# Optimization experiments

Hardware: AMD Instinct MI355X
Metric: run time of the kernel (lower is better)

Reference implementation:

```python
import jax, jax.numpy as jnp
import numpy as np

D = 768      # hidden_size
H = 12       # num_attention_heads
HD = D // H  # head_dim
F = 3072     # intermediate_size
B, S = 4, 2048
EPS = 1e-5


def _layer_norm(x, g, b):
    mu = jnp.mean(x, axis=-1, keepdims=True)
    var = jnp.mean(jnp.square(x - mu), axis=-1, keepdims=True)
    return (x - mu) * jax.lax.rsqrt(var + EPS) * g + b


def setup_inputs() -> dict:
    key = jax.random.key(0)
    ks = jax.random.split(key, 12)
    s_d = 1.0 / np.sqrt(D)
    s_f = 1.0 / np.sqrt(F)
    return {
        "x": jax.random.normal(ks[0], (B, S, D), jnp.float32),
        # per-head separate Q/K/V projections stacked along head axis [H, D, HD]
        "Wq": jax.random.normal(ks[1], (H, D, HD), jnp.float32) * s_d,
        "bq": jnp.zeros((H, HD), jnp.float32),
        "Wk": jax.random.normal(ks[2], (H, D, HD), jnp.float32) * s_d,
        "bk": jnp.zeros((H, HD), jnp.float32),
        "Wv": jax.random.normal(ks[3], (H, D, HD), jnp.float32) * s_d,
        "bv": jnp.zeros((H, HD), jnp.float32),
        "Wo": jax.random.normal(ks[4], (D, D), jnp.float32) * s_d,
        "bo": jnp.zeros((D,), jnp.float32),
        "W1": jax.random.normal(ks[5], (D, F), jnp.float32) * s_d,
        "b1": jnp.zeros((F,), jnp.float32),
        "W2": jax.random.normal(ks[6], (F, D), jnp.float32) * s_f,
        "b2": jnp.zeros((D,), jnp.float32),
        "g1": jnp.ones((D,), jnp.float32),
        "be1": jnp.zeros((D,), jnp.float32),
        "g2": jnp.ones((D,), jnp.float32),
        "be2": jnp.zeros((D,), jnp.float32),
    }


def reference(x, Wq, bq, Wk, bk, Wv, bv, Wo, bo, W1, b1, W2, b2, g1, be1, g2, be2):
    # NOTE: original module has NO residual connections; mask path is a no-op
    # (masked_fill is not in-place in the source), dropout is identity in eval.
    h = _layer_norm(x, g1, be1)
    # per-head projections: [B,H,S,HD]
    q = jnp.einsum('bsd,hde->bhse', h, Wq) + bq[None, :, None, :]
    k = jnp.einsum('bsd,hde->bhse', h, Wk) + bk[None, :, None, :]
    v = jnp.einsum('bsd,hde->bhse', h, Wv) + bv[None, :, None, :]
    scores = jnp.einsum('bhse,bhte->bhst', q, k) / jnp.sqrt(jnp.float32(HD))
    w = jax.nn.softmax(scores, axis=-1)          # [B,H,S,S]
    o = jnp.einsum('bhst,bhte->bhse', w, v)      # [B,H,S,HD]
    o = o.transpose(0, 2, 1, 3).reshape(B, S, D)  # concat heads along feature dim
    a = o @ Wo + bo
    h2 = _layer_norm(a, g2, be2)
    f = jax.nn.gelu(h2 @ W1 + b1, approximate=False)  # torch nn.GELU = exact erf
    return f @ W2 + b2
```

## Files before the change

### kernel.cpp

```cpp
#include <hip/hip_runtime.h>
#include <hip/hip_bf16.h>
#include <math.h>

typedef __hip_bfloat16 bf16;
typedef __attribute__((ext_vector_type(8))) short short8;
typedef __attribute__((ext_vector_type(4))) float f32x4;

#define D_  768
#define H_  12
#define HD_ 64
#define F_  3072
#define B_  4
#define S_  2048
#define BS_ (B_*S_)
#define SQK 1536
#define PSTR 72

__device__ __forceinline__ float b2f(bf16 x){ return __bfloat162float(x); }

union BU { bf16 b; unsigned short u; };
__device__ __forceinline__ bf16 f2b_fast(float x){
  BU t; t.u = (unsigned short)((__float_as_uint(x) + 0x8000u) >> 16); return t.b;
}
__device__ __forceinline__ unsigned pk2bf(float a, float b){
  return __builtin_amdgcn_perm(__float_as_uint(b) + 0x8000u,
                               __float_as_uint(a) + 0x8000u, 0x07060302u);
}

__device__ __forceinline__ f32x4 zero4(){ f32x4 z; z.x=0.f; z.y=0.f; z.z=0.f; z.w=0.f; return z; }

__device__ __forceinline__ f32x4 mfma16(uint4 a, uint4 b, f32x4 c){
  union U { uint4 u; short8 s; };
  U A, B; A.u = a; B.u = b;
  return __builtin_amdgcn_mfma_f32_16x16x32_bf16(A.s, B.s, c, 0, 0, 0);
}

typedef const __attribute__((address_space(1))) void gvoid;
typedef __attribute__((address_space(3))) void lvoid;
__device__ __forceinline__ void load_lds16(const void* g, void* l){
  __builtin_amdgcn_global_load_lds((gvoid*)g, (lvoid*)l, 16, 0, 0);
}

__device__ __forceinline__ float fast_gelu(float v){
  const float x = v * 0.70710678118654752f;
  const float ax = fabsf(x);
  const float t = __builtin_amdgcn_rcpf(fmaf(0.3275911f, ax, 1.0f));
  const float poly = t * fmaf(t, fmaf(t, fmaf(t, fmaf(t, 1.061405429f, -1.453152027f),
                                              1.421413741f), -0.284496736f), 0.254829592f);
  const float e = __builtin_amdgcn_exp2f(ax * ax * -1.4426950408889634f);
  const float erfax = 1.0f - poly * e;
  const float erfx = copysignf(erfax, x);
  return 0.5f * v * (1.0f + erfx);
}

__global__ __launch_bounds__(256)
void repack_t(const float* __restrict__ W, bf16* __restrict__ Wt, int K, int N)
{
  const int t = blockIdx.x * 256 + threadIdx.x;
  const int n = t % N;
  const int kg = t / N;
  const float* src = W + (size_t)kg * 8 * N + n;
  union { unsigned u32[4]; uint4 u; } pk;
#pragma unroll
  for (int j = 0; j < 4; ++j)
    pk.u32[j] = pk2bf(src[(size_t)(2 * j) * N], src[(size_t)(2 * j + 1) * N]);
  *(uint4*)(Wt + ((size_t)n * (K >> 3) + kg) * 8) = pk.u;
}

__global__ __launch_bounds__(256)
void repack_qkv_t(const float* __restrict__ Wq, const float* __restrict__ Wk,
                  const float* __restrict__ Wv, bf16* __restrict__ Wt)
{
  const int t = blockIdx.x * 256 + threadIdx.x;
  const int n = t % 2304;
  const int kg = t / 2304;
  const int sel = n / 768;
  const int nn = n - sel * 768;
  const int hh = nn >> 6;
  const int ee = nn & 63;
  const float* W = (sel == 0) ? Wq : (sel == 1) ? Wk : Wv;
  const float* src = W + ((size_t)hh * 768 + (size_t)kg * 8) * 64 + ee;
  union { unsigned u32[4]; uint4 u; } pk;
#pragma unroll
  for (int j = 0; j < 4; ++j)
    pk.u32[j] = pk2bf(src[(size_t)(2 * j) * 64], src[(size_t)(2 * j + 1) * 64]);
  *(uint4*)(Wt + ((size_t)n * 96 + kg) * 8) = pk.u;
}

__global__ __launch_bounds__(256)
void bias_qkv(const float* __restrict__ bq, const float* __restrict__ bk,
              const float* __restrict__ bv, float* __restrict__ out)
{
  const int t = blockIdx.x * 256 + threadIdx.x;
  out[t] = (t < 768) ? bq[t] : (t < 1536) ? bk[t - 768] : bv[t - 1536];
}

__global__ __launch_bounds__(256)
void ln_x_kernel(const float* __restrict__ X, const float* __restrict__ G,
                 const float* __restrict__ Bet, bf16* __restrict__ Y)
{
  const int t = threadIdx.x;
  const size_t row = blockIdx.x;
  const float* x = X + row * D_;
  float v0 = x[t], v1 = x[t + 256], v2 = x[t + 512];
  float s = v0 + v1 + v2;
#pragma unroll
  for (int d = 32; d >= 1; d >>= 1) s += __shfl_xor(s, d, 64);
  __shared__ float red[8];
  const int wv = t >> 6, ln = t & 63;
  if (ln == 0) red[wv] = s;
  __syncthreads();
  const float mu = (red[0] + red[1] + red[2] + red[3]) * (1.0f / 768.0f);
  const float d0 = v0 - mu, d1 = v1 - mu, d2 = v2 - mu;
  float sq = d0 * d0 + d1 * d1 + d2 * d2;
#pragma unroll
  for (int d = 32; d >= 1; d >>= 1) sq += __shfl_xor(sq, d, 64);
  if (ln == 0) red[4 + wv] = sq;
  __syncthreads();
  const float var = (red[4] + red[5] + red[6] + red[7]) * (1.0f / 768.0f);
  const float rs = rsqrtf(var + 1e-5f);
  bf16* y = Y + row * D_;
  y[t]       = f2b_fast(d0 * rs * G[t]       + Bet[t]);
  y[t + 256] = f2b_fast(d1 * rs * G[t + 256] + Bet[t + 256]);
  y[t + 512] = f2b_fast(d2 * rs * G[t + 512] + Bet[t + 512]);
}

__global__ __launch_bounds__(256)
void ln_h_kernel(const bf16* __restrict__ X, const float* __restrict__ G,
                 const float* __restrict__ Bet, bf16* __restrict__ Y)
{
  const int t = threadIdx.x;
  const size_t row = blockIdx.x;
  const bf16* x = X + row * D_;
  float v0 = b2f(x[t]), v1 = b2f(x[t + 256]), v2 = b2f(x[t + 512]);
  float s = v0 + v1 + v2;
#pragma unroll
  for (int d = 32; d >= 1; d >>= 1) s += __shfl_xor(s, d, 64);
  __shared__ float red[8];
  const int wv = t >> 6, ln = t & 63;
  if (ln == 0) red[wv] = s;
  __syncthreads();
  const float mu = (red[0] + red[1] + red[2] + red[3]) * (1.0f / 768.0f);
  const float d0 = v0 - mu, d1 = v1 - mu, d2 = v2 - mu;
  float sq = d0 * d0 + d1 * d1 + d2 * d2;
#pragma unroll
  for (int d = 32; d >= 1; d >>= 1) sq += __shfl_xor(sq, d, 64);
  if (ln == 0) red[4 + wv] = sq;
  __syncthreads();
  const float var = (red[4] + red[5] + red[6] + red[7]) * (1.0f / 768.0f);
  const float rs = rsqrtf(var + 1e-5f);
  bf16* y = Y + row * D_;
  y[t]       = f2b_fast(d0 * rs * G[t]       + Bet[t]);
  y[t + 256] = f2b_fast(d1 * rs * G[t + 256] + Bet[t + 256]);
  y[t + 512] = f2b_fast(d2 * rs * G[t + 512] + Bet[t + 512]);
}

__global__ __launch_bounds__(256)
void gemm_lds(const bf16* __restrict__ A, const bf16* __restrict__ Wt,
              const float* __restrict__ bias, bf16* __restrict__ C,
              bf16* __restrict__ Vp, float* __restrict__ Cf,
              int K, int N, int mode)
{
  __shared__ __align__(16) bf16 As[2][128 * 32];
  __shared__ __align__(16) bf16 Bs[2][128 * 32];

  const int tid = threadIdx.x;
  const int wave = tid >> 6, lane = tid & 63;
  const int l15 = lane & 15, qd = lane >> 4;
  const int wy = wave >> 1, wx = wave & 1;

  int id = (int)blockIdx.y * (int)gridDim.x + (int)blockIdx.x;
  const int chunk = ((int)gridDim.x * (int)gridDim.y) >> 3;
  id = (id & 7) * chunk + (id >> 3);
  const int bx = id % (int)gridDim.x;
  const int by = id / (int)gridDim.x;

  const size_t m0 = (size_t)by * 128;
  const int n0 = bx * 128;

  const int r0 = tid >> 2, c0 = tid & 3;
  const int c0s = c0 ^ ((r0 >> 1) & 3);
  const bf16* Ag0 = A  + (m0 + r0) * (size_t)K + c0s * 8;
  const bf16* Ag1 = A  + (m0 + r0 + 64) * (size_t)K + c0s * 8;
  const bf16* Bg0 = Wt + (size_t)(n0 + r0) * K + c0s * 8;
  const bf16* Bg1 = Wt + (size_t)(n0 + r0 + 64) * K + c0s * 8;

  f32x4 acc[4][4];
#pragma unroll
  for (int i = 0; i < 4; ++i)
#pragma unroll
    for (int j = 0; j < 4; ++j) acc[i][j] = zero4();

  const int arow = wy * 64;
  const int brow = wx * 64;
  const int ksw = (l15 >> 1) & 3;

  load_lds16(Ag0, &As[0][(size_t)tid * 8]);
  load_lds16(Ag1, &As[0][(size_t)(tid + 256) * 8]);
  load_lds16(Bg0, &Bs[0][(size_t)tid * 8]);
  load_lds16(Bg1, &Bs[0][(size_t)(tid + 256) * 8]);
  __syncthreads();

  for (int k0 = 0; k0 < K; k0 += 32) {
    const int cur = (k0 >> 5) & 1;
    if (k0 + 32 < K) {
      const int nxt = cur ^ 1;
      load_lds16(Ag0 + k0 + 32, &As[nxt][(size_t)tid * 8]);
      load_lds16(Ag1 + k0 + 32, &As[nxt][(size_t)(tid + 256) * 8]);
      load_lds16(Bg0 + k0 + 32, &Bs[nxt][(size_t)tid * 8]);
      load_lds16(Bg1 + k0 + 32, &Bs[nxt][(size_t)(tid + 256) * 8]);
    }
    uint4 af[4], bfr[4];
#pragma unroll
    for (int mt = 0; mt < 4; ++mt)
      af[mt] = *(const uint4*)(&As[cur][0] + (size_t)(arow + mt * 16 + l15) * 32 + (qd ^ ksw) * 8);
#pragma unroll
    for (int nt = 0; nt < 4; ++nt)
      bfr[nt] = *(const uint4*)(&Bs[cur][0] + (size_t)(brow + nt * 16 + l15) * 32 + (qd ^ ksw) * 8);
#pragma unroll
    for (int nt = 0; nt < 4; ++nt)
#pragma unroll
      for (int mt = 0; mt < 4; ++mt)
        acc[nt][mt] = mfma16(bfr[nt], af[mt], acc[nt][mt]);
    __syncthreads();
  }

  const size_t wm0 = m0 + arow;
  const int wn0 = n0 + brow;
#pragma unroll
  for (int nt = 0; nt < 4; ++nt) {
    const int nb = wn0 + nt * 16 + qd * 4;
    const f32x4 bs4 = *(const f32x4*)(bias + nb);
#pragma unroll
    for (int mt = 0; mt < 4; ++mt) {
      const size_t m = wm0 + mt * 16 + l15;
      float v[4];
#pragma unroll
      for (int r = 0; r < 4; ++r) v[r] = acc[nt][mt][r] + bs4[r];
      if (mode == 2) {
#pragma unroll
        for (int r = 0; r < 4; ++r) v[r] = fast_gelu(v[r]);
      }
      if (mode == 3) {
        f32x4 o; o.x = v[0]; o.y = v[1]; o.z = v[2]; o.w = v[3];
        *(f32x4*)(Cf + m * (size_t)N + nb) = o;
      } else if (mode == 0) {
        if (nb < SQK) {
          uint2 w; w.x = pk2bf(v[0], v[1]); w.y = pk2bf(v[2], v[3]);
          *(uint2*)(C + m * SQK + nb) = w;
        } else {
          const int bb = (int)(m >> 11);
          const int ss = (int)(m & 2047);
          const int hh = (nb - SQK) >> 6;
          const size_t vbase = (((size_t)bb * H_ + hh) * 256 + (ss >> 3)) * 512 + (ss & 7);
#pragma unroll
          for (int r = 0; r < 4; ++r)
            Vp[vbase + (size_t)((nb & 63) + r) * 8] = f2b_fast(v[r]);
        }
      } else {
        uint2 w; w.x = pk2bf(v[0], v[1]); w.y = pk2bf(v[2], v[3]);
        *(uint2*)(C + m * (size_t)N + nb) = w;
      }
    }
  }
}

__global__ __launch_bounds__(256)
void gemm_lds64(const bf16* __restrict__ A, const bf16* __restrict__ Wt,
                const float* __restrict__ bias, bf16* __restrict__ C,
                float* __restrict__ Cf, int K, int N, int mode)
{
  __shared__ __align__(16) bf16 As[2][128 * 32];
  __shared__ __align__(16) bf16 Bs[2][64 * 32];

  const int tid = threadIdx.x;
  const int wave = tid >> 6, lane = tid & 63;
  const int l15 = lane & 15, qd = lane >> 4;

  int id = (int)blockIdx.y * (int)gridDim.x + (int)blockIdx.x;
  const int chunk = ((int)gridDim.x * (int)gridDim.y) >> 3;
  id = (id & 7) * chunk + (id >> 3);
  const int bx = id % (int)gridDim.x;
  const int by = id / (int)gridDim.x;

  const size_t m0 = (size_t)by * 128;
  const int n0 = bx * 64;

  const int r0 = tid >> 2, c0 = tid & 3;
  const int c0s = c0 ^ ((r0 >> 1) & 3);
  const bf16* Ag0 = A  + (m0 + r0) * (size_t)K + c0s * 8;
  const bf16* Ag1 = A  + (m0 + r0 + 64) * (size_t)K + c0s * 8;
  const bf16* Bg0 = Wt + (size_t)(n0 + r0) * K + c0s * 8;

  f32x4 acc[4][2];
#pragma unroll
  for (int i = 0; i < 4; ++i)
#pragma unroll
    for (int j = 0; j < 2; ++j) acc[i][j] = zero4();

  const int arow = wave * 32;
  const int ksw = (l15 >> 1) & 3;

  load_lds16(Ag0, &As[0][(size_t)tid * 8]);
  load_lds16(Ag1, &As[0][(size_t)(tid + 256) * 8]);
  load_lds16(Bg0, &Bs[0][(size_t)tid * 8]);
  __syncthreads();

  for (int k0 = 0; k0 < K; k0 += 32) {
    const int cur = (k0 >> 5) & 1;
    if (k0 + 32 < K) {
      const int nxt = cur ^ 1;
      load_lds16(Ag0 + k0 + 32, &As[nxt][(size_t)tid * 8]);
      load_lds16(Ag1 + k0 + 32, &As[nxt][(size_t)(tid + 256) * 8]);
      load_lds16(Bg0 + k0 + 32, &Bs[nxt][(size_t)tid * 8]);
    }
    uint4 af[2], bfr[4];
#pragma unroll
    for (int mt = 0; mt < 2; ++mt)
      af[mt] = *(const uint4*)(&As[cur][0] + (size_t)(arow + mt * 16 + l15) * 32 + (qd ^ ksw) * 8);
#pragma unroll
    for (int nt = 0; nt < 4; ++nt)
      bfr[nt] = *(const uint4*)(&Bs[cur][0] + (size_t)(nt * 16 + l15) * 32 + (qd ^ ksw) * 8);
#pragma unroll
    for (int nt = 0; nt < 4; ++nt)
#pragma unroll
      for (int mt = 0; mt < 2; ++mt)
        acc[nt][mt] = mfma16(bfr[nt], af[mt], acc[nt][mt]);
    __syncthreads();
  }

  const size_t wm0 = m0 + arow;
#pragma unroll
  for (int nt = 0; nt < 4; ++nt) {
    const int nb = n0 + nt * 16 + qd * 4;
    const f32x4 bs4 = *(const f32x4*)(bias + nb);
#pragma unroll
    for (int mt = 0; mt < 2; ++mt) {
      const size_t m = wm0 + mt * 16 + l15;
      float v[4];
#pragma unroll
      for (int r = 0; r < 4; ++r) v[r] = acc[nt][mt][r] + bs4[r];
      if (mode == 3) {
        f32x4 o; o.x = v[0]; o.y = v[1]; o.z = v[2]; o.w = v[3];
        *(f32x4*)(Cf + m * (size_t)N + nb) = o;
      } else {
        uint2 w; w.x = pk2bf(v[0], v[1]); w.y = pk2bf(v[2], v[3]);
        *(uint2*)(C + m * (size_t)N + nb) = w;
      }
    }
  }
}

__global__ __launch_bounds__(256, 3)
void attn_kernel(const bf16* __restrict__ QK, const bf16* __restrict__ Vp,
                 bf16* __restrict__ O)
{
  const int tid  = threadIdx.x;
  const int wave = tid >> 6;
  const int lane = tid & 63;
  const int l15 = lane & 15;
  const int qd  = lane >> 4;

  int bid = blockIdx.y * gridDim.x + blockIdx.x;
  bid = (bid & 7) * 96 + (bid >> 3);
  const int bh = bid >> 4;
  const int b  = bh / H_;
  const int h  = bh % H_;
  const int q0 = (bid & 15) * 128 + wave * 32;

  const bf16* Qb = QK + (size_t)b * S_ * SQK + h * HD_;
  const bf16* Kb = Qb + D_;
  const bf16* Vb = Vp + (size_t)bh * 256 * 512;

  __shared__ __align__(16) bf16 Ks[2][64 * 64];
  __shared__ __align__(16) bf16 Vs[2][8 * 512];
  __shared__ __align__(16) unsigned short Pl[4][32 * PSTR];
  unsigned short* Pw = &Pl[wave][0];

  const int srow = tid >> 3;
  const int sch  = (tid & 7) ^ (srow & 7);
  const bf16* Kst = Kb + (size_t)srow * SQK + sch * 8;
  const bf16* Vst = Vb + tid * 8;

  uint4 qf[2][2];
#pragma unroll
  for (int mt = 0; mt < 2; ++mt)
#pragma unroll
    for (int ks = 0; ks < 2; ++ks)
      qf[mt][ks] = *(const uint4*)(Qb + (size_t)(q0 + mt * 16 + l15) * SQK + ks * 32 + qd * 8);

  f32x4 o_[2][5];
#pragma unroll
  for (int mt = 0; mt < 2; ++mt)
#pragma unroll
    for (int dt = 0; dt < 5; ++dt) o_[mt][dt] = zero4();

  uint4 vones;
  { const unsigned v = (l15 == 0) ? 0x3F803F80u : 0u; vones.x = v; vones.y = v; vones.z = v; vones.w = v; }

  const float C1 = 1.4426950408889634f * 0.125f;
  const float C0 = -12.0f * 1.4426950408889634f;

  load_lds16(Kst,                      &Ks[0][tid * 8]);
  load_lds16(Kst + (size_t)32 * SQK,   &Ks[0][2048 + tid * 8]);
  load_lds16(Vst,                      &Vs[0][tid * 8]);
  load_lds16(Vst + 2048,               &Vs[0][2048 + tid * 8]);
  __syncthreads();

  for (int sk = 0; sk < S_; sk += 64) {
    const int cur = (sk >> 6) & 1;
    const bf16* Ksc = &Ks[cur][0];
    const bf16* Vsc = &Vs[cur][0];

    uint4 kf[4][2];
#pragma unroll
    for (int kt = 0; kt < 4; ++kt)
#pragma unroll
      for (int ks = 0; ks < 2; ++ks)
        kf[kt][ks] = *(const uint4*)(Ksc + (size_t)(kt * 16 + l15) * 64
                                         + ((ks * 4 + qd) ^ (l15 & 7)) * 8);
    uint4 vf[2][4];
#pragma unroll
    for (int ks = 0; ks < 2; ++ks)
#pragma unroll
      for (int dt = 0; dt < 4; ++dt)
        vf[ks][dt] = *(const uint4*)(Vsc + (ks * 4 + qd) * 512 + (dt * 16 + l15) * 8);

    if (sk + 64 < S_) {
      const int nxt = cur ^ 1;
      const bf16* Kn = Kst + (size_t)(sk + 64) * SQK;
      const bf16* Vn = Vst + (size_t)(sk + 64) * 64;
      load_lds16(Kn,                    &Ks[nxt][tid * 8]);
      load_lds16(Kn + (size_t)32 * SQK, &Ks[nxt][2048 + tid * 8]);
      load_lds16(Vn,                    &Vs[nxt][tid * 8]);
      load_lds16(Vn + 2048,             &Vs[nxt][2048 + tid * 8]);
    }

    f32x4 st[4][2];
#pragma unroll
    for (int kt = 0; kt < 4; ++kt)
#pragma unroll
      for (int mt = 0; mt < 2; ++mt) st[kt][mt] = zero4();
    __builtin_amdgcn_s_setprio(1);
#pragma unroll
    for (int ks = 0; ks < 2; ++ks)
#pragma unroll
      for (int kt = 0; kt < 4; ++kt)
#pragma unroll
        for (int mt = 0; mt < 2; ++mt)
          st[kt][mt] = mfma16(kf[kt][ks], qf[mt][ks], st[kt][mt]);
    __builtin_amdgcn_s_setprio(0);

#pragma unroll
    for (int mt = 0; mt < 2; ++mt) {
      unsigned short* prow = Pw + (mt * 16 + l15) * PSTR;
#pragma unroll
      for (int kt = 0; kt < 4; ++kt) {
        const float p0 = __builtin_amdgcn_exp2f(fmaf(st[kt][mt][0], C1, C0));
        const float p1 = __builtin_amdgcn_exp2f(fmaf(st[kt][mt][1], C1, C0));
        const float p2 = __builtin_amdgcn_exp2f(fmaf(st[kt][mt][2], C1, C0));
        const float p3 = __builtin_amdgcn_exp2f(fmaf(st[kt][mt][3], C1, C0));
        uint2 w; w.x = pk2bf(p0, p1); w.y = pk2bf(p2, p3);
        *(uint2*)(prow + kt * 16 + qd * 4) = w;
      }
    }

    uint4 pf[2][2];
#pragma unroll
    for (int mt = 0; mt < 2; ++mt)
#pragma unroll
      for (int ks = 0; ks < 2; ++ks)
        pf[mt][ks] = *(const uint4*)(Pw + (mt * 16 + l15) * PSTR + ks * 32 + qd * 8);

    __builtin_amdgcn_s_setprio(1);
#pragma unroll
    for (int ks = 0; ks < 2; ++ks)
#pragma unroll
      for (int mt = 0; mt < 2; ++mt) {
#pragma unroll
        for (int dt = 0; dt < 4; ++dt)
          o_[mt][dt] = mfma16(pf[mt][ks], vf[ks][dt], o_[mt][dt]);
        o_[mt][4] = mfma16(pf[mt][ks], vones, o_[mt][4]);
      }
    __builtin_amdgcn_s_setprio(0);

    __syncthreads();
  }

  const size_t tok0 = (size_t)b * S_ + q0;
#pragma unroll
  for (int mt = 0; mt < 2; ++mt) {
#pragma unroll
    for (int r = 0; r < 4; ++r) {
      const float lr = __shfl(o_[mt][4][r], (lane & 48), 64);
      const float inv = __builtin_amdgcn_rcpf(lr);
      const size_t row = tok0 + mt * 16 + qd * 4 + r;
#pragma unroll
      for (int dt = 0; dt < 4; ++dt)
        O[row * D_ + h * HD_ + dt * 16 + l15] = f2b_fast(o_[mt][dt][r] * inv);
    }
  }
}

extern "C" void kernel_launch(void* const* d_in, const int* in_sizes, int n_in,
                              void* d_out, int out_size, void* d_ws, size_t ws_size,
                              hipStream_t stream)
{
  const float* x   = (const float*)d_in[0];
  const float* Wq  = (const float*)d_in[1];
  const float* bq  = (const float*)d_in[2];
  const float* Wk  = (const float*)d_in[3];
  const float* bk  = (const float*)d_in[4];
  const float* Wv  = (const float*)d_in[5];
  const float* bv  = (const float*)d_in[6];
  const float* Wo  = (const float*)d_in[7];
  const float* bo  = (const float*)d_in[8];
  const float* W1  = (const float*)d_in[9];
  const float* b1  = (const float*)d_in[10];
  const float* W2  = (const float*)d_in[11];
  const float* b2  = (const float*)d_in[12];
  const float* g1  = (const float*)d_in[13];
  const float* be1 = (const float*)d_in[14];
  const float* g2  = (const float*)d_in[15];
  const float* be2 = (const float*)d_in[16];

  const bool full = ws_size >= (size_t)77079552;

  char* ws = (char*)d_ws;
  bf16* qk     = (bf16*)(ws + 0);
  bf16* vp     = (bf16*)(ws + 25165824);
  bf16* h1     = (bf16*)(ws + 37748736);
  bf16* obuf   = h1;
  bf16* abuf   = (bf16*)(ws + 0);
  bf16* h2     = (bf16*)(ws + (full ? 50331648u : 25165824u));
  bf16* fbuf   = (bf16*)(ws + 0);
  const size_t wb = full ? 62914560u : 50331648u;
  bf16* wqkv_p = (bf16*)(ws + wb);
  bf16* wo_p   = (bf16*)(ws + wb + 3538944u);
  bf16* w1_p   = (bf16*)(ws + wb + 4718592u);
  bf16* w2_p   = (bf16*)(ws + wb + 9437184u);
  float* bqkvf = (float*)(ws + wb + 14155776u);

  float* outp = (float*)d_out;

  repack_qkv_t<<<dim3(864),  dim3(256), 0, stream>>>(Wq, Wk, Wv, wqkv_p);
  repack_t    <<<dim3(288),  dim3(256), 0, stream>>>(Wo, wo_p, 768, 768);
  repack_t    <<<dim3(1152), dim3(256), 0, stream>>>(W1, w1_p, 768, 3072);
  repack_t    <<<dim3(1152), dim3(256), 0, stream>>>(W2, w2_p, 3072, 768);
  bias_qkv    <<<dim3(9),    dim3(256), 0, stream>>>(bq, bk, bv, bqkvf);

  ln_x_kernel<<<dim3(BS_), dim3(256), 0, stream>>>(x, g1, be1, h1);
  gemm_lds<<<dim3(18, 64), dim3(256), 0, stream>>>(h1, wqkv_p, bqkvf, qk, vp, nullptr, 768, 2304, 0);
  attn_kernel<<<dim3(16, 48), dim3(256), 0, stream>>>(qk, vp, obuf);
  gemm_lds64<<<dim3(12, 64), dim3(256), 0, stream>>>(obuf, wo_p, bo, abuf, nullptr, 768, 768, 1);
  ln_h_kernel<<<dim3(BS_), dim3(256), 0, stream>>>(abuf, g2, be2, h2);

  if (full) {
    gemm_lds<<<dim3(24, 64), dim3(256), 0, stream>>>(h2, w1_p, b1, fbuf, nullptr, nullptr, 768, 3072, 2);
    gemm_lds64<<<dim3(12, 64), dim3(256), 0, stream>>>(fbuf, w2_p, b2, nullptr, outp, 3072, 768, 3);
  } else {
    gemm_lds<<<dim3(24, 32), dim3(256), 0, stream>>>(h2, w1_p, b1, fbuf, nullptr, nullptr, 768, 3072, 2);
    gemm_lds64<<<dim3(12, 32), dim3(256), 0, stream>>>(fbuf, w2_p, b2, nullptr, outp, 3072, 768, 3);
    gemm_lds<<<dim3(24, 32), dim3(256), 0, stream>>>(h2 + (size_t)4096 * D_, w1_p, b1, fbuf, nullptr, nullptr, 768, 3072, 2);
    gemm_lds64<<<dim3(12, 32), dim3(256), 0, stream>>>(fbuf, w2_p, b2, nullptr, outp + (size_t)4096 * D_, 3072, 768, 3);
  }
}
```

Baseline: 421.0 us.

## Deepen K-tile to 64 in narrow GEMM and hoist LDS fragment reads before prefetch

The 128x64 GEMM kernel now stages 64-wide K slices per iteration instead of 32, using an 8-chunk XOR swizzle and double-buffered shared memory that is twice as large. This halves the number of barrier-separated iterations and issues more MFMAs per sync. In both GEMM kernels the LDS fragment reads are moved ahead of the next-tile global-to-LDS prefetch so they are not queued behind it. The larger shared footprint may reduce occupancy.

```diff
diff --git a/kernel.cpp b/kernel.cpp
--- a/kernel.cpp
+++ b/kernel.cpp
@@ -203,6 +203,13 @@
 
   for (int k0 = 0; k0 < K; k0 += 32) {
     const int cur = (k0 >> 5) & 1;
+    uint4 af[4], bfr[4];
+#pragma unroll
+    for (int mt = 0; mt < 4; ++mt)
+      af[mt] = *(const uint4*)(&As[cur][0] + (size_t)(arow + mt * 16 + l15) * 32 + (qd ^ ksw) * 8);
+#pragma unroll
+    for (int nt = 0; nt < 4; ++nt)
+      bfr[nt] = *(const uint4*)(&Bs[cur][0] + (size_t)(brow + nt * 16 + l15) * 32 + (qd ^ ksw) * 8);
     if (k0 + 32 < K) {
       const int nxt = cur ^ 1;
       load_lds16(Ag0 + k0 + 32, &As[nxt][(size_t)tid * 8]);
@@ -210,13 +217,6 @@
       load_lds16(Bg0 + k0 + 32, &Bs[nxt][(size_t)tid * 8]);
       load_lds16(Bg1 + k0 + 32, &Bs[nxt][(size_t)(tid + 256) * 8]);
     }
-    uint4 af[4], bfr[4];
-#pragma unroll
-    for (int mt = 0; mt < 4; ++mt)
-      af[mt] = *(const uint4*)(&As[cur][0] + (size_t)(arow + mt * 16 + l15) * 32 + (qd ^ ksw) * 8);
-#pragma unroll
-    for (int nt = 0; nt < 4; ++nt)
-      bfr[nt] = *(const uint4*)(&Bs[cur][0] + (size_t)(brow + nt * 16 + l15) * 32 + (qd ^ ksw) * 8);
 #pragma unroll
     for (int nt = 0; nt < 4; ++nt)
 #pragma unroll
@@ -270,8 +270,8 @@
                 const float* __restrict__ bias, bf16* __restrict__ C,
                 float* __restrict__ Cf, int K, int N, int mode)
 {
-  __shared__ __align__(16) bf16 As[2][128 * 32];
-  __shared__ __align__(16) bf16 Bs[2][64 * 32];
+  __shared__ __align__(16) bf16 As[2][128 * 64];
+  __shared__ __align__(16) bf16 Bs[2][64 * 64];
 
   const int tid = threadIdx.x;
   const int wave = tid >> 6, lane = tid & 63;
@@ -286,11 +286,10 @@
   const size_t m0 = (size_t)by * 128;
   const int n0 = bx * 64;
 
-  const int r0 = tid >> 2, c0 = tid & 3;
-  const int c0s = c0 ^ ((r0 >> 1) & 3);
-  const bf16* Ag0 = A  + (m0 + r0) * (size_t)K + c0s * 8;
-  const bf16* Ag1 = A  + (m0 + r0 + 64) * (size_t)K + c0s * 8;
-  const bf16* Bg0 = Wt + (size_t)(n0 + r0) * K + c0s * 8;
+  const int srow = tid >> 3;
+  const int sch  = (tid & 7) ^ (srow & 7);
+  const bf16* Ag = A  + (m0 + srow) * (size_t)K + sch * 8;
+  const bf16* Bg = Wt + (size_t)(n0 + srow) * K + sch * 8;
 
   f32x4 acc[4][2];
 #pragma unroll
@@ -299,33 +298,47 @@
     for (int j = 0; j < 2; ++j) acc[i][j] = zero4();
 
   const int arow = wave * 32;
-  const int ksw = (l15 >> 1) & 3;
-
-  load_lds16(Ag0, &As[0][(size_t)tid * 8]);
-  load_lds16(Ag1, &As[0][(size_t)(tid + 256) * 8]);
-  load_lds16(Bg0, &Bs[0][(size_t)tid * 8]);
-  __syncthreads();
-
-  for (int k0 = 0; k0 < K; k0 += 32) {
-    const int cur = (k0 >> 5) & 1;
-    if (k0 + 32 < K) {
+  const int ksw = l15 & 7;
+
+#pragma unroll
+  for (int p = 0; p < 4; ++p)
+    load_lds16(Ag + (size_t)32 * p * K, &As[0][(size_t)(tid + 256 * p) * 8]);
+#pragma unroll
+  for (int p = 0; p < 2; ++p)
+    load_lds16(Bg + (size_t)32 * p * K, &Bs[0][(size_t)(tid + 256 * p) * 8]);
+  __syncthreads();
+
+  for (int k0 = 0; k0 < K; k0 += 64) {
+    const int cur = (k0 >> 6) & 1;
+    uint4 af[2][2], bfr[4][2];
+#pragma unroll
+    for (int mt = 0; mt < 2; ++mt)
+#pragma unroll
+      for (int ks = 0; ks < 2; ++ks)
+        af[mt][ks] = *(const uint4*)(&As[cur][0]
+                       + (size_t)(arow + mt * 16 + l15) * 64 + ((ks * 4 + qd) ^ ksw) * 8);
+#pragma unroll
+    for (int nt = 0; nt < 4; ++nt)
+#pragma unroll
+      for (int ks = 0; ks < 2; ++ks)
+        bfr[nt][ks] = *(const uint4*)(&Bs[cur][0]
+                       + (size_t)(nt * 16 + l15) * 64 + ((ks * 4 + qd) ^ ksw) * 8);
+    if (k0 + 64 < K) {
       const int nxt = cur ^ 1;
-      load_lds16(Ag0 + k0 + 32, &As[nxt][(size_t)tid * 8]);
-      load_lds16(Ag1 + k0 + 32, &As[nxt][(size_t)(tid + 256) * 8]);
-      load_lds16(Bg0 + k0 + 32, &Bs[nxt][(size_t)tid * 8]);
-    }
-    uint4 af[2], bfr[4];
-#pragma unroll
-    for (int mt = 0; mt < 2; ++mt)
-      af[mt] = *(const uint4*)(&As[cur][0] + (size_t)(arow + mt * 16 + l15) * 32 + (qd ^ ksw) * 8);
-#pragma unroll
-    for (int nt = 0; nt < 4; ++nt)
-      bfr[nt] = *(const uint4*)(&Bs[cur][0] + (size_t)(nt * 16 + l15) * 32 + (qd ^ ksw) * 8);
-#pragma unroll
-    for (int nt = 0; nt < 4; ++nt)
-#pragma unroll
-      for (int mt = 0; mt < 2; ++mt)
-        acc[nt][mt] = mfma16(bfr[nt], af[mt], acc[nt][mt]);
+#pragma unroll
+      for (int p = 0; p < 4; ++p)
+        load_lds16(Ag + (size_t)32 * p * K + k0 + 64, &As[nxt][(size_t)(tid + 256 * p) * 8]);
+#pragma unroll
+      for (int p = 0; p < 2; ++p)
+        load_lds16(Bg + (size_t)32 * p * K + k0 + 64, &Bs[nxt][(size_t)(tid + 256 * p) * 8]);
+    }
+#pragma unroll
+    for (int ks = 0; ks < 2; ++ks)
+#pragma unroll
+      for (int nt = 0; nt < 4; ++nt)
+#pragma unroll
+        for (int mt = 0; mt < 2; ++mt)
+          acc[nt][mt] = mfma16(bfr[nt][ks], af[mt][ks], acc[nt][mt]);
     __syncthreads();
   }
 
```

Result: faster. 397.8 us, median of 2 (-5.5%).
